# Kernel tuning notes

Measured on AMD Instinct MI355X. Metric: run time of the kernel, lower is better.

The kernel has to match this reference:

```python
import jax, jax.numpy as jnp
import numpy as np

# dims: D=embed_dim (= number of experts), H=heads, P=image patches, Q=query embeddings, B=batch
D, H, N, P, B, Q = 256, 8, 256, 1024, 1, 64
HD = D // H
EPS = 1e-5


def _ln(x, g, b):
    m = x.mean(-1, keepdims=True)
    v = x.var(-1, keepdims=True)
    return (x - m) / jnp.sqrt(v + EPS) * g + b


def _mha(q_x, kv_x, Wqkv, bqkv, Wo, bo):
    # standard torch nn.MultiheadAttention (batch_first, eval mode)
    Wq, Wk, Wv = jnp.split(Wqkv, 3, axis=0)
    bq, bk, bv = jnp.split(bqkv, 3, axis=0)
    q = q_x @ Wq.T + bq
    k = kv_x @ Wk.T + bk
    v = kv_x @ Wv.T + bv
    Bq, S, _ = q.shape
    Sk = k.shape[1]
    qh = q.reshape(Bq, S, H, HD)
    kh = k.reshape(Bq, Sk, H, HD)
    vh = v.reshape(Bq, Sk, H, HD)
    att = jax.nn.softmax(jnp.einsum('bqhd,bkhd->bhqk', qh, kh) / np.sqrt(HD).astype(np.float32), axis=-1)
    ctx = jnp.einsum('bhqk,bkhd->bqhd', att, vh).reshape(Bq, S, D)
    return ctx @ Wo.T + bo


def setup_inputs() -> dict:
    key = jax.random.key(0)
    ks = jax.random.split(key, 12)
    s = 0.02  # weight init scale
    return {
        'image_patches': jax.random.normal(ks[0], (B, P, D), jnp.float32),
        'expert_tokens': jax.random.normal(ks[1], (B, N, D), jnp.float32),
        'query_embeddings': jax.random.normal(ks[2], (B, Q, D), jnp.float32),
        'Wqkv_experts': jax.random.normal(ks[3], (N, 3 * D, D), jnp.float32) * s,
        'bqkv_experts': jnp.zeros((N, 3 * D), jnp.float32),
        'Wo_experts': jax.random.normal(ks[4], (N, D, D), jnp.float32) * s,
        'bo_experts': jnp.zeros((N, D), jnp.float32),
        'Wqkv_q': jax.random.normal(ks[5], (3 * D, D), jnp.float32) * s,
        'bqkv_q': jnp.zeros((3 * D,), jnp.float32),
        'Wo_q': jax.random.normal(ks[6], (D, D), jnp.float32) * s,
        'bo_q': jnp.zeros((D,), jnp.float32),
        'Wqkv_s': jax.random.normal(ks[7], (3 * D, D), jnp.float32) * s,
        'bqkv_s': jnp.zeros((3 * D,), jnp.float32),
        'Wo_s': jax.random.normal(ks[8], (D, D), jnp.float32) * s,
        'bo_s': jnp.zeros((D,), jnp.float32),
        'W1': jax.random.normal(ks[9], (4 * D, D), jnp.float32) * s,
        'b1': jnp.zeros((4 * D,), jnp.float32),
        'W2': jax.random.normal(ks[10], (D, 4 * D), jnp.float32) * s,
        'b2': jnp.zeros((D,), jnp.float32),
        'ln1_g': jnp.ones((D,), jnp.float32), 'ln1_b': jnp.zeros((D,), jnp.float32),
        'ln2_g': jnp.ones((D,), jnp.float32), 'ln2_b': jnp.zeros((D,), jnp.float32),
        'ln3_g': jnp.ones((D,), jnp.float32), 'ln3_b': jnp.zeros((D,), jnp.float32),
    }


def reference(image_patches, expert_tokens, query_embeddings,
              Wqkv_experts, bqkv_experts, Wo_experts, bo_experts,
              Wqkv_q, bqkv_q, Wo_q, bo_q,
              Wqkv_s, bqkv_s, Wo_s, bo_s,
              W1, b1, W2, b2,
              ln1_g, ln1_b, ln2_g, ln2_b, ln3_g, ln3_b):
    # --- per-expert cross attention (the embed_dim separate MHA calls, fused/batched) ---
    Wq, Wk, Wv = jnp.split(Wqkv_experts, 3, axis=1)   # each [N, D, D]
    bq, bk, bv = jnp.split(bqkv_experts, 3, axis=1)   # each [N, D]
    q = jnp.einsum('bnd,ned->bne', expert_tokens, Wq) + bq                       # [B,N,D]
    K = jnp.einsum('bpd,ned->bnpe', image_patches, Wk) + bk[None, :, None, :]    # [B,N,P,D]
    V = jnp.einsum('bpd,ned->bnpe', image_patches, Wv) + bv[None, :, None, :]    # [B,N,P,D]
    qh = q.reshape(B, N, H, HD)
    Kh = K.reshape(B, N, P, H, HD)
    Vh = V.reshape(B, N, P, H, HD)
    att = jax.nn.softmax(jnp.einsum('bnhd,bnphd->bnhp', qh, Kh) / np.sqrt(HD).astype(np.float32), axis=-1)
    image_attention_weights = att.mean(axis=2)        # [B,N,P] head-averaged, torch default
    ctx = jnp.einsum('bnhp,bnphd->bnhd', att, Vh).reshape(B, N, D)
    attended_image = jnp.einsum('bnd,ned->bne', ctx, Wo_experts) + bo_experts    # [B,N,D]
    attended_image = _ln(attended_image + expert_tokens, ln1_g, ln1_b)
    # --- query cross attention ---
    attended_query = _mha(attended_image, query_embeddings, Wqkv_q, bqkv_q, Wo_q, bo_q)
    attended_query = _ln(attended_query + attended_image, ln2_g, ln2_b)
    # --- FFN (no residual in original) ---
    expert_refined = jax.nn.relu(attended_query @ W1.T + b1) @ W2.T + b2
    # --- expert self attention + residual + norm ---
    sa = _mha(expert_refined, expert_refined, Wqkv_s, bqkv_s, Wo_s, bo_s)
    expert_features = _ln(sa + expert_refined, ln3_g, ln3_b)
    return expert_features, image_attention_weights
```

## Files before the change

kernel.cpp:

```cpp
#include <hip/hip_runtime.h>

#define DD 256
#define NH 8
#define NP 1024
#define NQ 64
#define SCALE 0.17677669529663687f

typedef float f32x4v __attribute__((ext_vector_type(4)));
typedef __bf16 bfv8 __attribute__((ext_vector_type(8)));

union BF8 { bfv8 v; unsigned short u16[8]; uint4 q; };

__device__ __forceinline__ float wred_sum(float p) {
  #pragma unroll
  for (int m = 32; m; m >>= 1) p += __shfl_xor(p, m);
  return p;
}
__device__ __forceinline__ float wred_max(float p) {
  #pragma unroll
  for (int m = 32; m; m >>= 1) p = fmaxf(p, __shfl_xor(p, m));
  return p;
}
__device__ __forceinline__ float red8(float p) {
  p += __shfl_xor(p, 1);
  p += __shfl_xor(p, 2);
  p += __shfl_xor(p, 4);
  return p;
}
__device__ __forceinline__ float dot4(float4 a, float4 b) {
  return a.x*b.x + a.y*b.y + a.z*b.z + a.w*b.w;
}
__device__ __forceinline__ unsigned short f2b(float f) {
  unsigned int u = __float_as_uint(f);
  u += 0x7fffu + ((u >> 16) & 1u);
  return (unsigned short)(u >> 16);
}
__device__ __forceinline__ BF8 cvt8(float4 a, float4 b) {
  BF8 r;
  r.u16[0]=f2b(a.x); r.u16[1]=f2b(a.y); r.u16[2]=f2b(a.z); r.u16[3]=f2b(a.w);
  r.u16[4]=f2b(b.x); r.u16[5]=f2b(b.y); r.u16[6]=f2b(b.z); r.u16[7]=f2b(b.w);
  return r;
}
__device__ __forceinline__ f32x4v mfma16(BF8 a, BF8 b, f32x4v c) {
  return __builtin_amdgcn_mfma_f32_16x16x32_bf16(a.v, b.v, c, 0, 0, 0);
}
__device__ __forceinline__ float2 b2f2(unsigned int u) {
  return make_float2(__uint_as_float(u << 16), __uint_as_float(u & 0xffff0000u));
}
__device__ __forceinline__ float dotb8(uint4 w, float4 x0, float4 x1) {
  float2 p0 = b2f2(w.x), p1 = b2f2(w.y), p2 = b2f2(w.z), p3 = b2f2(w.w);
  return p0.x*x0.x + p0.y*x0.y + p1.x*x0.z + p1.y*x0.w
       + p2.x*x1.x + p2.y*x1.y + p3.x*x1.z + p3.y*x1.w;
}

__device__ __forceinline__ void preload8(const float* x, int lane, float4* xf) {
  const int o = (lane & 7) * 4;
  #pragma unroll
  for (int cc = 0; cc < 8; ++cc) xf[cc] = *(const float4*)&x[cc*32 + o];
}
__device__ __forceinline__ void pass16(const float* __restrict__ W, int ldk,
                                       int r0, int lane, const float4* xf,
                                       float* outA, float* outB) {
  const float* baseA = W + (size_t)(r0 + (lane >> 3))*ldk + (lane & 7)*4;
  const float* baseB = baseA + (size_t)8*ldk;
  float4 wa[8], wb[8];
  #pragma unroll
  for (int cc = 0; cc < 8; ++cc) wa[cc] = *(const float4*)&baseA[cc*32];
  #pragma unroll
  for (int cc = 0; cc < 8; ++cc) wb[cc] = *(const float4*)&baseB[cc*32];
  float a = 0.f, b = 0.f;
  #pragma unroll
  for (int cc = 0; cc < 8; ++cc) { a += dot4(wa[cc], xf[cc]); b += dot4(wb[cc], xf[cc]); }
  *outA = red8(a); *outB = red8(b);
}
__device__ __forceinline__ void preload8b(const float* x, int lane, float4* xf) {
  const int o = (lane & 7) * 8;
  #pragma unroll
  for (int cc = 0; cc < 4; ++cc) {
    xf[2*cc]   = *(const float4*)&x[cc*64 + o];
    xf[2*cc+1] = *(const float4*)&x[cc*64 + o + 4];
  }
}
__device__ __forceinline__ void pass16b(const unsigned short* __restrict__ W, int ldk,
                                        int r0, int lane, const float4* xf,
                                        float* outA, float* outB) {
  const unsigned short* baseA = W + (size_t)(r0 + (lane >> 3))*ldk + (lane & 7)*8;
  const unsigned short* baseB = baseA + (size_t)8*ldk;
  uint4 wa[4], wb[4];
  #pragma unroll
  for (int cc = 0; cc < 4; ++cc) wa[cc] = *(const uint4*)&baseA[cc*64];
  #pragma unroll
  for (int cc = 0; cc < 4; ++cc) wb[cc] = *(const uint4*)&baseB[cc*64];
  float a = 0.f, b = 0.f;
  #pragma unroll
  for (int cc = 0; cc < 4; ++cc) {
    a += dotb8(wa[cc], xf[2*cc], xf[2*cc+1]);
    b += dotb8(wb[cc], xf[2*cc], xf[2*cc+1]);
  }
  *outA = red8(a); *outB = red8(b);
}

__device__ __forceinline__ void layernorm_store(const float* buf, float* outp,
                                                const float* g, const float* b,
                                                float* red, int tid, int wid, int lane)
{
  __syncthreads();
  if (wid == 0) {
    float s = buf[lane] + buf[lane+64] + buf[lane+128] + buf[lane+192];
    s = wred_sum(s);
    if (!lane) red[0] = s * (1.f/256.f);
  }
  __syncthreads();
  float mn = red[0];
  if (wid == 0) {
    float d0 = buf[lane]-mn, d1 = buf[lane+64]-mn, d2 = buf[lane+128]-mn, d3 = buf[lane+192]-mn;
    float s = d0*d0 + d1*d1 + d2*d2 + d3*d3;
    s = wred_sum(s);
    if (!lane) red[1] = rsqrtf(s * (1.f/256.f) + 1e-5f);
  }
  __syncthreads();
  if (tid < 256) outp[tid] = (buf[tid] - mn) * red[1] * g[tid] + b[tid];
}

__global__ __launch_bounds__(256)
void k_pre(const float* __restrict__ patches, uint4* __restrict__ pTB,
           uint4* __restrict__ patchesB,
           const float* __restrict__ qe, const float* __restrict__ Wqkv_q,
           const float* __restrict__ bqkv_q, float* __restrict__ kvq,
           const float* __restrict__ Wo_q, const float* __restrict__ W1,
           const float* __restrict__ W2, const float* __restrict__ Wqkv_s,
           unsigned short* __restrict__ wsB)
{
  const int b = blockIdx.x, tid = threadIdx.x;
  if (b < 128) {
    const int T = b*4 + (tid >> 6), l = tid & 63;
    const int kt = T >> 6, nt = T & 63;
    const int row = nt*16 + (l & 15), col = kt*32 + (l >> 4)*8;
    float4 a = *(const float4*)&patches[(size_t)row*DD + col];
    float4 c = *(const float4*)&patches[(size_t)row*DD + col + 4];
    pTB[(size_t)T*64 + l] = cvt8(a, c).q;
  } else if (b < 256) {
    const int T = (b - 128)*4 + (tid >> 6), l = tid & 63;
    const int kt = T >> 4, nt = T & 15;
    const int col = nt*16 + (l & 15), p0 = kt*32 + (l >> 4)*8;
    float v[8];
    #pragma unroll
    for (int j = 0; j < 8; ++j) v[j] = patches[(size_t)(p0 + j)*DD + col];
    BF8 r;
    #pragma unroll
    for (int j = 0; j < 8; ++j) r.u16[j] = f2b(v[j]);
    patchesB[(size_t)T*64 + l] = r.q;
  } else if (b < 320) {
    __shared__ float x[DD], kvrow[512];
    const int j = b - 256, w = tid >> 6, lane = tid & 63;
    if (tid < DD) x[tid] = qe[j*DD + tid];
    __syncthreads();
    float4 xf[8]; preload8(x, lane, xf);
    #pragma unroll
    for (int g = 0; g < 8; ++g) {
      int r0 = w*128 + g*16;
      float a, bb;
      pass16(Wqkv_q + (size_t)DD*DD, DD, r0, lane, xf, &a, &bb);
      int rA = r0 + (lane >> 3);
      if ((lane & 7) == 0) {
        kvrow[rA]   = a  + bqkv_q[DD + rA];
        kvrow[rA+8] = bb + bqkv_q[DD + rA + 8];
      }
    }
    __syncthreads();
    kvq[(size_t)j*512 + tid]       = kvrow[tid];
    kvq[(size_t)j*512 + 256 + tid] = kvrow[256 + tid];
  } else {
    const int gid = (b - 320)*256 + tid;
    const float* src;
    size_t dof;
    if      (gid < 8192)  { src = Wqkv_q + (size_t)gid*8;           dof = (size_t)gid*8; }
    else if (gid < 16384) { src = Wo_q   + (size_t)(gid-8192)*8;    dof = 65536  + (size_t)(gid-8192)*8; }
    else if (gid < 49152) { src = W1     + (size_t)(gid-16384)*8;   dof = 131072 + (size_t)(gid-16384)*8; }
    else if (gid < 81920) { src = W2     + (size_t)(gid-49152)*8;   dof = 393216 + (size_t)(gid-49152)*8; }
    else                  { src = Wqkv_s + (size_t)(gid-81920)*8;   dof = 655360 + (size_t)(gid-81920)*8; }
    float4 a = *(const float4*)&src[0];
    float4 c = *(const float4*)&src[4];
    *(uint4*)&wsB[dof] = cvt8(a, c).q;
  }
}

__global__ __launch_bounds__(256)
void k_qt(const float* __restrict__ et_g, const float* __restrict__ Wqkv_e,
          const float* __restrict__ bqkv_e, float* __restrict__ t_ws)
{
  const int b = blockIdx.x, n = b >> 2, hh = b & 3;
  const int tid = threadIdx.x, w = tid >> 6, lane = tid & 63;
  __shared__ float x[DD], qL[64], tpart[4][DD];
  const float* Wn = Wqkv_e + (size_t)n*(3*DD*DD);
  const float* bn = bqkv_e + (size_t)n*(3*DD);
  if (tid < DD) x[tid] = et_g[(size_t)n*DD + tid];
  __syncthreads();
  {
    float4 xf[8]; preload8(x, lane, xf);
    float a, bq;
    pass16(Wn, DD, hh*64 + w*16, lane, xf, &a, &bq);
    int rL = w*16 + (lane >> 3);
    if ((lane & 7) == 0) {
      qL[rL]   = a  + bn[hh*64 + rL];
      qL[rL+8] = bq + bn[hh*64 + rL + 8];
    }
  }
  __syncthreads();
  {
    const float* Wk = Wn + (size_t)DD*DD + (size_t)(hh*64 + w*16)*DD;
    float4 acc = make_float4(0.f, 0.f, 0.f, 0.f);
    #pragma unroll
    for (int r = 0; r < 16; ++r) {
      float qs = qL[w*16 + r];
      float4 wv = *(const float4*)&Wk[(size_t)r*DD + 4*lane];
      acc.x += qs*wv.x; acc.y += qs*wv.y; acc.z += qs*wv.z; acc.w += qs*wv.w;
    }
    *(float4*)&tpart[w][4*lane] = acc;
  }
  __syncthreads();
  {
    float tA = tpart[0][tid] + tpart[1][tid];
    float tB = tpart[2][tid] + tpart[3][tid];
    t_ws[(size_t)n*2048 + (size_t)(2*hh)*DD + tid]     = tA;
    t_ws[(size_t)n*2048 + (size_t)(2*hh+1)*DD + tid]   = tB;
  }
}

__global__ __launch_bounds__(512)
void k_mid1(const float* __restrict__ t_ws,
            const uint4* __restrict__ pTB, const uint4* __restrict__ patchesB,
            float* __restrict__ u_ws, float* __restrict__ iaw)
{
  const int n = blockIdx.x, tid = threadIdx.x, w = tid >> 6, lane = tid & 63;
  __shared__ float attS[NH][NP];
  __shared__ __align__(16) uint4 attB[16][128];
  __shared__ float tS[16][260];
  __shared__ float uS[NH][DD];

  for (int idx = tid; idx < 2048; idx += 512) tS[idx >> 8][idx & 255] = t_ws[(size_t)n*2048 + idx];
  __syncthreads();

  BF8 afr[8];
  {
    const int rr = lane & 15, ko = (lane >> 4)*8;
    #pragma unroll
    for (int kt = 0; kt < 8; ++kt) {
      float4 a = *(const float4*)&tS[rr][kt*32 + ko];
      float4 c = *(const float4*)&tS[rr][kt*32 + ko + 4];
      afr[kt] = cvt8(a, c);
    }
  }
  {
    #pragma unroll
    for (int t8 = 0; t8 < 8; ++t8) {
      const int nt = w*8 + t8;
      f32x4v acc = {0.f, 0.f, 0.f, 0.f};
      #pragma unroll
      for (int kt = 0; kt < 8; ++kt) {
        BF8 bb; bb.q = pTB[(size_t)(kt*64 + nt)*64 + lane];
        acc = mfma16(afr[kt], bb, acc);
      }
      if (lane < 32) {
        const int r0 = (lane >> 4)*4, cc = nt*16 + (lane & 15);
        #pragma unroll
        for (int i = 0; i < 4; ++i) attS[r0 + i][cc] = acc[i];
      }
    }
  }
  __syncthreads();
  {
    const int h = w;
    float v[16];
    #pragma unroll
    for (int k = 0; k < 16; ++k) v[k] = attS[h][k*64 + lane] * SCALE;
    float mx = v[0];
    #pragma unroll
    for (int k = 1; k < 16; ++k) mx = fmaxf(mx, v[k]);
    mx = wred_max(mx);
    float sum = 0.f;
    #pragma unroll
    for (int k = 0; k < 16; ++k) { v[k] = __expf(v[k] - mx); sum += v[k]; }
    sum = wred_sum(sum);
    float rinv = 1.f / sum;
    #pragma unroll
    for (int k = 0; k < 16; ++k) attS[h][k*64 + lane] = v[k] * rinv;
  }
  __syncthreads();
  #pragma unroll
  for (int rep = 0; rep < 2; ++rep) {
    int p = rep*512 + tid;
    float s = 0.f;
    #pragma unroll
    for (int h = 0; h < NH; ++h) s += attS[h][p];
    iaw[(size_t)n*NP + p] = s * 0.125f;
  }
  #pragma unroll
  for (int rep = 0; rep < 2; ++rep) {
    int C = rep*512 + tid;
    int row = C >> 7, c = C & 127;
    float4 a = *(const float4*)&attS[row][c*8];
    float4 b = *(const float4*)&attS[row][c*8 + 4];
    int swz = (c & ~7) | ((c ^ row) & 7);
    attB[row][swz] = cvt8(a, b).q;
  }
  __syncthreads();
  {
    const int nt0 = 2*w, nt1 = 2*w + 1;
    f32x4v acc0 = {0.f,0.f,0.f,0.f}, acc1 = {0.f,0.f,0.f,0.f};
    const int rr = lane & 15, cq = lane >> 4;
    #pragma unroll 8
    for (int kt = 0; kt < 32; ++kt) {
      int cc = kt*4 + cq;
      int swz = (cc & ~7) | ((cc ^ rr) & 7);
      BF8 a;  a.q  = attB[rr][swz];
      BF8 b0; b0.q = patchesB[(size_t)(kt*16 + nt0)*64 + lane];
      BF8 b1; b1.q = patchesB[(size_t)(kt*16 + nt1)*64 + lane];
      acc0 = mfma16(a, b0, acc0);
      acc1 = mfma16(a, b1, acc1);
    }
    if (lane < 32) {
      const int r0 = (lane >> 4)*4;
      #pragma unroll
      for (int i = 0; i < 4; ++i) {
        uS[r0+i][nt0*16 + (lane & 15)] = acc0[i];
        uS[r0+i][nt1*16 + (lane & 15)] = acc1[i];
      }
    }
  }
  __syncthreads();
  for (int idx = tid; idx < 2048; idx += 512) u_ws[(size_t)n*2048 + idx] = (&uS[0][0])[idx];
}

__global__ __launch_bounds__(256)
void k_ctx(const float* __restrict__ u_ws, const float* __restrict__ Wqkv_e,
           const float* __restrict__ bqkv_e, float* __restrict__ ctx_ws)
{
  const int b = blockIdx.x, n = b >> 2, qt = b & 3;
  const int tid = threadIdx.x, w = tid >> 6, lane = tid & 63;
  const float* Wn = Wqkv_e + (size_t)n*(3*DD*DD);
  const float* bn = bqkv_e + (size_t)n*(3*DD);
  const int head = qt*2 + (w >> 1);
  float4 xf[8]; preload8(u_ws + (size_t)n*2048 + (size_t)head*DD, lane, xf);
  float a, bq;
  pass16(Wn + (size_t)2*DD*DD, DD, qt*64 + w*16, lane, xf, &a, &bq);
  int rA = qt*64 + w*16 + (lane >> 3);
  if ((lane & 7) == 0) {
    ctx_ws[(size_t)n*DD + rA]     = a  + bn[2*DD + rA];
    ctx_ws[(size_t)n*DD + rA + 8] = bq + bn[2*DD + rA + 8];
  }
}

__global__ __launch_bounds__(256)
void k_out(const float* __restrict__ ctx_ws, const float* __restrict__ et_g,
           const float* __restrict__ Wo_e, const float* __restrict__ bo_e,
           float* __restrict__ res_ws)
{
  const int b = blockIdx.x, n = b >> 2, qt = b & 3;
  const int tid = threadIdx.x, w = tid >> 6, lane = tid & 63;
  __shared__ float cx[DD];
  if (tid < DD) cx[tid] = ctx_ws[(size_t)n*DD + tid];
  __syncthreads();
  float4 xf[8]; preload8(cx, lane, xf);
  float a, bq;
  pass16(Wo_e + (size_t)n*DD*DD, DD, qt*64 + w*16, lane, xf, &a, &bq);
  int rA = qt*64 + w*16 + (lane >> 3);
  if ((lane & 7) == 0) {
    res_ws[(size_t)n*DD + rA]     = a  + bo_e[(size_t)n*DD + rA]     + et_g[(size_t)n*DD + rA];
    res_ws[(size_t)n*DD + rA + 8] = bq + bo_e[(size_t)n*DD + rA + 8] + et_g[(size_t)n*DD + rA + 8];
  }
}

__global__ __launch_bounds__(1024)
void k_tail(const float* __restrict__ res_ws, const float* __restrict__ kvq,
            const unsigned short* __restrict__ wsB,
            const float* __restrict__ bqkv_q, const float* __restrict__ bo_q,
            const float* __restrict__ b1, const float* __restrict__ b2,
            const float* __restrict__ bqkv_s,
            const float* __restrict__ ln1g, const float* __restrict__ ln1b,
            const float* __restrict__ ln2g, const float* __restrict__ ln2b,
            float* __restrict__ er_g, float* __restrict__ qkvs_g)
{
  const int n = blockIdx.x, tid = threadIdx.x, w = tid >> 6, lane = tid & 63;
  __shared__ float xL[DD], qL[DD], ctxL[DD], resS[DD], attq[NH][NQ], red2[2];
  __shared__ float hb[1024], qrow[768];
  const unsigned short* WqB  = wsB;
  const unsigned short* WoqB = wsB + 65536;
  const unsigned short* W1B  = wsB + 131072;
  const unsigned short* W2B  = wsB + 393216;
  const unsigned short* WsB  = wsB + 655360;

  if (tid < DD) resS[tid] = res_ws[(size_t)n*DD + tid];
  layernorm_store(resS, xL, ln1g, ln1b, red2, tid, w, lane);
  __syncthreads();

  {
    float4 xf[8]; preload8b(xL, lane, xf);
    float a, b;
    pass16b(WqB, DD, w*16, lane, xf, &a, &b);
    int rA = w*16 + (lane >> 3);
    if ((lane & 7) == 0) { qL[rA] = a + bqkv_q[rA]; qL[rA+8] = b + bqkv_q[rA+8]; }
  }
  __syncthreads();
  if (w < 8) {
    const int h = w, j = lane;
    float4 q4[8];
    #pragma unroll
    for (int m = 0; m < 8; ++m) q4[m] = *(const float4*)&qL[h*32 + 4*m];
    const float* kj = kvq + (size_t)j*512 + h*32;
    float s = 0.f;
    #pragma unroll
    for (int m = 0; m < 8; ++m) s += dot4(*(const float4*)&kj[4*m], q4[m]);
    s *= SCALE;
    float mx = wred_max(s);
    float p = __expf(s - mx);
    float sum = wred_sum(p);
    attq[h][j] = p / sum;
  }
  __syncthreads();
  if (tid < DD) {
    const int rr = tid, h = rr >> 5;
    float acc = 0.f;
    #pragma unroll 4
    for (int j4 = 0; j4 < 16; ++j4) {
      float4 a4 = *(const float4*)&attq[h][j4*4];
      acc += a4.x * kvq[(size_t)(j4*4+0)*512 + DD + rr]
           + a4.y * kvq[(size_t)(j4*4+1)*512 + DD + rr]
           + a4.z * kvq[(size_t)(j4*4+2)*512 + DD + rr]
           + a4.w * kvq[(size_t)(j4*4+3)*512 + DD + rr];
    }
    ctxL[rr] = acc;
  }
  __syncthreads();
  {
    float4 xf[8]; preload8b(ctxL, lane, xf);
    float a, b;
    pass16b(WoqB, DD, w*16, lane, xf, &a, &b);
    int rA = w*16 + (lane >> 3);
    if ((lane & 7) == 0) { resS[rA] = a + bo_q[rA] + xL[rA]; resS[rA+8] = b + bo_q[rA+8] + xL[rA+8]; }
  }
  layernorm_store(resS, xL, ln2g, ln2b, red2, tid, w, lane);
  __syncthreads();

  {
    float4 xf[8]; preload8b(xL, lane, xf);
    #pragma unroll
    for (int g = 0; g < 4; ++g) {
      int r0 = w*64 + g*16;
      float a, b;
      pass16b(W1B, DD, r0, lane, xf, &a, &b);
      int rA = r0 + (lane >> 3);
      if ((lane & 7) == 0) { hb[rA] = fmaxf(a + b1[rA], 0.f); hb[rA+8] = fmaxf(b + b1[rA+8], 0.f); }
    }
  }
  __syncthreads();
  {
    float accA = 0.f, accB = 0.f;
    #pragma unroll
    for (int kc = 0; kc < 4; ++kc) {
      float4 xh[8]; preload8b(hb + kc*256, lane, xh);
      float a, b;
      pass16b(W2B + kc*256, 1024, w*16, lane, xh, &a, &b);
      accA += a; accB += b;
    }
    int rA = w*16 + (lane >> 3);
    if ((lane & 7) == 0) { qL[rA] = accA + b2[rA]; qL[rA+8] = accB + b2[rA+8]; }
  }
  __syncthreads();
  {
    float4 xf[8]; preload8b(qL, lane, xf);
    #pragma unroll
    for (int g = 0; g < 3; ++g) {
      int r0 = w*48 + g*16;
      float a, b;
      pass16b(WsB, DD, r0, lane, xf, &a, &b);
      int rA = r0 + (lane >> 3);
      if ((lane & 7) == 0) { qrow[rA] = a + bqkv_s[rA]; qrow[rA+8] = b + bqkv_s[rA+8]; }
    }
  }
  __syncthreads();
  if (tid < 768) qkvs_g[(size_t)n*768 + tid] = qrow[tid];
  if (tid < DD)  er_g[(size_t)n*DD + tid]   = qL[tid];
}

__global__ __launch_bounds__(1024)
void k_sa(const float* __restrict__ er, const float* __restrict__ qkvs,
          const float* __restrict__ Wo_s, const float* __restrict__ bo_s,
          const float* __restrict__ ln3g, const float* __restrict__ ln3b,
          float* __restrict__ ef)
{
  const int i = blockIdx.x, tid = threadIdx.x, w = tid >> 6, lane = tid & 63;
  __shared__ float x[DD], attl[NH][256], ctxp[4][DD], resS[DD], red2[2];
  if (tid < DD) x[tid] = er[(size_t)i*DD + tid];
  {
    const int h = w & 7, kh = w >> 3;
    float4 q4[8];
    #pragma unroll
    for (int m = 0; m < 8; ++m) q4[m] = *(const float4*)&qkvs[(size_t)i*768 + h*32 + 4*m];
    #pragma unroll
    for (int rep = 0; rep < 2; ++rep) {
      int j = kh*128 + rep*64 + lane;
      const float* kj = qkvs + (size_t)j*768 + DD + h*32;
      float4 k4[8];
      #pragma unroll
      for (int m = 0; m < 8; ++m) k4[m] = *(const float4*)&kj[4*m];
      float s = 0.f;
      #pragma unroll
      for (int m = 0; m < 8; ++m) s += dot4(k4[m], q4[m]);
      attl[h][j] = s * SCALE;
    }
  }
  __syncthreads();
  if (w < 8) {
    const int h = w;
    float v0 = attl[h][lane], v1 = attl[h][lane+64], v2 = attl[h][lane+128], v3 = attl[h][lane+192];
    float mx = wred_max(fmaxf(fmaxf(v0,v1), fmaxf(v2,v3)));
    float e0 = __expf(v0-mx), e1 = __expf(v1-mx), e2 = __expf(v2-mx), e3 = __expf(v3-mx);
    float sum = wred_sum(e0+e1+e2+e3);
    float r = 1.f/sum;
    attl[h][lane] = e0*r; attl[h][lane+64] = e1*r; attl[h][lane+128] = e2*r; attl[h][lane+192] = e3*r;
  }
  __syncthreads();
  {
    const int rr = tid & 255, qtr = tid >> 8, h = rr >> 5;
    float acc = 0.f;
    #pragma unroll 4
    for (int j4 = qtr*16; j4 < qtr*16 + 16; ++j4) {
      float4 a4 = *(const float4*)&attl[h][j4*4];
      acc += a4.x * qkvs[(size_t)(j4*4+0)*768 + 512 + rr]
           + a4.y * qkvs[(size_t)(j4*4+1)*768 + 512 + rr]
           + a4.z * qkvs[(size_t)(j4*4+2)*768 + 512 + rr]
           + a4.w * qkvs[(size_t)(j4*4+3)*768 + 512 + rr];
    }
    ctxp[qtr][rr] = acc;
  }
  __syncthreads();
  {
    float4 xf[8];
    const int o = (lane & 7)*4;
    #pragma unroll
    for (int cc = 0; cc < 8; ++cc) {
      float4 a = *(const float4*)&ctxp[0][cc*32 + o];
      float4 b = *(const float4*)&ctxp[1][cc*32 + o];
      float4 c = *(const float4*)&ctxp[2][cc*32 + o];
      float4 d = *(const float4*)&ctxp[3][cc*32 + o];
      xf[cc] = make_float4(a.x+b.x+c.x+d.x, a.y+b.y+c.y+d.y,
                           a.z+b.z+c.z+d.z, a.w+b.w+c.w+d.w);
    }
    float a, b;
    pass16(Wo_s, DD, w*16, lane, xf, &a, &b);
    int rA = w*16 + (lane >> 3);
    if ((lane & 7) == 0) { resS[rA] = a + bo_s[rA] + x[rA]; resS[rA+8] = b + bo_s[rA+8] + x[rA+8]; }
  }
  layernorm_store(resS, ef + (size_t)i*DD, ln3g, ln3b, red2, tid, w, lane);
}

extern "C" void kernel_launch(void* const* d_in, const int* in_sizes, int n_in,
                              void* d_out, int out_size, void* d_ws, size_t ws_size,
                              hipStream_t stream) {
  const float* patches = (const float*)d_in[0];
  const float* et      = (const float*)d_in[1];
  const float* qe      = (const float*)d_in[2];
  const float* Wqkv_e  = (const float*)d_in[3];
  const float* bqkv_e  = (const float*)d_in[4];
  const float* Wo_e    = (const float*)d_in[5];
  const float* bo_e    = (const float*)d_in[6];
  const float* Wqkv_q  = (const float*)d_in[7];
  const float* bqkv_q  = (const float*)d_in[8];
  const float* Wo_q    = (const float*)d_in[9];
  const float* bo_q    = (const float*)d_in[10];
  const float* Wqkv_s  = (const float*)d_in[11];
  const float* bqkv_s  = (const float*)d_in[12];
  const float* Wo_s    = (const float*)d_in[13];
  const float* bo_s    = (const float*)d_in[14];
  const float* W1      = (const float*)d_in[15];
  const float* b1      = (const float*)d_in[16];
  const float* W2      = (const float*)d_in[17];
  const float* b2      = (const float*)d_in[18];
  const float* ln1g = (const float*)d_in[19]; const float* ln1b = (const float*)d_in[20];
  const float* ln2g = (const float*)d_in[21]; const float* ln2b = (const float*)d_in[22];
  const float* ln3g = (const float*)d_in[23]; const float* ln3b = (const float*)d_in[24];

  float* ef  = (float*)d_out;
  float* iaw = (float*)d_out + 65536;

  float* ws           = (float*)d_ws;
  uint4* pTB          = (uint4*)ws;
  uint4* patchesB     = (uint4*)(ws + 131072);
  float* kvq          = ws + 262144;
  float* t_ws         = ws + 294912;
  float* u_ws         = ws + 819200;
  float* ctx_ws       = ws + 1343488;
  float* res_ws       = ws + 1409024;
  float* er           = ws + 1474560;
  float* qkvs         = ws + 1540096;
  unsigned short* wsB = (unsigned short*)(ws + 1736704);

  k_pre<<<736, 256, 0, stream>>>(patches, pTB, patchesB, qe, Wqkv_q, bqkv_q, kvq,
                                 Wo_q, W1, W2, Wqkv_s, wsB);
  k_qt<<<1024, 256, 0, stream>>>(et, Wqkv_e, bqkv_e, t_ws);
  k_mid1<<<256, 512, 0, stream>>>(t_ws, pTB, patchesB, u_ws, iaw);
  k_ctx<<<1024, 256, 0, stream>>>(u_ws, Wqkv_e, bqkv_e, ctx_ws);
  k_out<<<1024, 256, 0, stream>>>(ctx_ws, et, Wo_e, bo_e, res_ws);
  k_tail<<<256, 1024, 0, stream>>>(res_ws, kvq, wsB, bqkv_q, bo_q, b1, b2, bqkv_s,
                                   ln1g, ln1b, ln2g, ln2b, er, qkvs);
  k_sa<<<256, 1024, 0, stream>>>(er, qkvs, Wo_s, bo_s, ln3g, ln3b, ef);
}
```

Baseline: 145.9 us.

## Fuse expert q/t, attention and ctx kernels into one two-block-per-expert kernel

Merges k_qt, k_mid1 and k_ctx into a single k_front2 kernel. Each expert is split across two 512-thread blocks, one per group of four heads, so the t and u intermediates stay in shared memory instead of going through global workspace. Shared memory is reused through an aliased buffer, and the head-averaged attention weights are written as per-half partials that k_tail combines. This removes two kernel launches and the global round trips, at the cost of some wasted MFMA rows (only 4 of 16 used) and an extra partial-sum pass.

```diff
diff --git a/kernel.cpp b/kernel.cpp
--- a/kernel.cpp
+++ b/kernel.cpp
@@ -185,60 +185,59 @@
   }
 }
 
-__global__ __launch_bounds__(256)
-void k_qt(const float* __restrict__ et_g, const float* __restrict__ Wqkv_e,
-          const float* __restrict__ bqkv_e, float* __restrict__ t_ws)
+__global__ __launch_bounds__(512, 4)
+void k_front2(const float* __restrict__ et_g,
+              const float* __restrict__ Wqkv_e, const float* __restrict__ bqkv_e,
+              const uint4* __restrict__ pTB, const uint4* __restrict__ patchesB,
+              float* __restrict__ ctx_ws, float* __restrict__ iawp)
 {
-  const int b = blockIdx.x, n = b >> 2, hh = b & 3;
+  const int blk = blockIdx.x, n = blk >> 1, half = blk & 1;
   const int tid = threadIdx.x, w = tid >> 6, lane = tid & 63;
-  __shared__ float x[DD], qL[64], tpart[4][DD];
+  __shared__ __align__(16) char big[32768];
+  __shared__ float attS[4][NP];
+  __shared__ float uS[4][DD];
+  __shared__ float xL[DD], qL[128];
+  float (*tpart)[256] = (float (*)[256])big;
+  float (*tS)[260]    = (float (*)[260])(big + 8192);
+  uint4 (*attB)[128]  = (uint4 (*)[128])big;
+
   const float* Wn = Wqkv_e + (size_t)n*(3*DD*DD);
   const float* bn = bqkv_e + (size_t)n*(3*DD);
-  if (tid < DD) x[tid] = et_g[(size_t)n*DD + tid];
-  __syncthreads();
-  {
-    float4 xf[8]; preload8(x, lane, xf);
+
+  if (tid < DD) xL[tid] = et_g[(size_t)n*DD + tid];
+  __syncthreads();
+
+  {
+    float4 xf[8]; preload8(xL, lane, xf);
     float a, bq;
-    pass16(Wn, DD, hh*64 + w*16, lane, xf, &a, &bq);
+    pass16(Wn, DD, half*128 + w*16, lane, xf, &a, &bq);
     int rL = w*16 + (lane >> 3);
     if ((lane & 7) == 0) {
-      qL[rL]   = a  + bn[hh*64 + rL];
-      qL[rL+8] = bq + bn[hh*64 + rL + 8];
-    }
-  }
-  __syncthreads();
-  {
-    const float* Wk = Wn + (size_t)DD*DD + (size_t)(hh*64 + w*16)*DD;
+      qL[rL]   = a  + bn[half*128 + rL];
+      qL[rL+8] = bq + bn[half*128 + rL + 8];
+    }
+  }
+  __syncthreads();
+
+  {
+    const int hl = w >> 1, dh = w & 1;
+    const float* Wk = Wn + (size_t)DD*DD + (size_t)(half*128 + hl*32 + dh*16)*DD;
     float4 acc = make_float4(0.f, 0.f, 0.f, 0.f);
     #pragma unroll
     for (int r = 0; r < 16; ++r) {
-      float qs = qL[w*16 + r];
+      float qs = qL[hl*32 + dh*16 + r];
       float4 wv = *(const float4*)&Wk[(size_t)r*DD + 4*lane];
       acc.x += qs*wv.x; acc.y += qs*wv.y; acc.z += qs*wv.z; acc.w += qs*wv.w;
     }
     *(float4*)&tpart[w][4*lane] = acc;
   }
   __syncthreads();
-  {
-    float tA = tpart[0][tid] + tpart[1][tid];
-    float tB = tpart[2][tid] + tpart[3][tid];
-    t_ws[(size_t)n*2048 + (size_t)(2*hh)*DD + tid]     = tA;
-    t_ws[(size_t)n*2048 + (size_t)(2*hh+1)*DD + tid]   = tB;
-  }
-}
-
-__global__ __launch_bounds__(512)
-void k_mid1(const float* __restrict__ t_ws,
-            const uint4* __restrict__ pTB, const uint4* __restrict__ patchesB,
-            float* __restrict__ u_ws, float* __restrict__ iaw)
-{
-  const int n = blockIdx.x, tid = threadIdx.x, w = tid >> 6, lane = tid & 63;
-  __shared__ float attS[NH][NP];
-  __shared__ __align__(16) uint4 attB[16][128];
-  __shared__ float tS[16][260];
-  __shared__ float uS[NH][DD];
-
-  for (int idx = tid; idx < 2048; idx += 512) tS[idx >> 8][idx & 255] = t_ws[(size_t)n*2048 + idx];
+  #pragma unroll
+  for (int rep = 0; rep < 2; ++rep) {
+    int idx = rep*512 + tid;
+    int hl = idx >> 8, c = idx & 255;
+    tS[hl][c] = tpart[2*hl][c] + tpart[2*hl+1][c];
+  }
   __syncthreads();
 
   BF8 afr[8];
@@ -261,19 +260,20 @@
         BF8 bb; bb.q = pTB[(size_t)(kt*64 + nt)*64 + lane];
         acc = mfma16(afr[kt], bb, acc);
       }
-      if (lane < 32) {
-        const int r0 = (lane >> 4)*4, cc = nt*16 + (lane & 15);
+      if (lane < 16) {
+        const int cc = nt*16 + lane;
         #pragma unroll
-        for (int i = 0; i < 4; ++i) attS[r0 + i][cc] = acc[i];
+        for (int i = 0; i < 4; ++i) attS[i][cc] = acc[i];
       }
     }
   }
   __syncthreads();
-  {
-    const int h = w;
+
+  if (w < 4) {
+    const int hl = w;
     float v[16];
     #pragma unroll
-    for (int k = 0; k < 16; ++k) v[k] = attS[h][k*64 + lane] * SCALE;
+    for (int k = 0; k < 16; ++k) v[k] = attS[hl][k*64 + lane] * SCALE;
     float mx = v[0];
     #pragma unroll
     for (int k = 1; k < 16; ++k) mx = fmaxf(mx, v[k]);
@@ -284,27 +284,25 @@
     sum = wred_sum(sum);
     float rinv = 1.f / sum;
     #pragma unroll
-    for (int k = 0; k < 16; ++k) attS[h][k*64 + lane] = v[k] * rinv;
-  }
-  __syncthreads();
+    for (int k = 0; k < 16; ++k) attS[hl][k*64 + lane] = v[k] * rinv;
+  }
+  __syncthreads();
+
   #pragma unroll
   for (int rep = 0; rep < 2; ++rep) {
     int p = rep*512 + tid;
-    float s = 0.f;
-    #pragma unroll
-    for (int h = 0; h < NH; ++h) s += attS[h][p];
-    iaw[(size_t)n*NP + p] = s * 0.125f;
-  }
-  #pragma unroll
-  for (int rep = 0; rep < 2; ++rep) {
-    int C = rep*512 + tid;
-    int row = C >> 7, c = C & 127;
+    float s = attS[0][p] + attS[1][p] + attS[2][p] + attS[3][p];
+    iawp[(size_t)blk*NP + p] = s;
+  }
+  {
+    int row = tid >> 7, c = tid & 127;
     float4 a = *(const float4*)&attS[row][c*8];
     float4 b = *(const float4*)&attS[row][c*8 + 4];
     int swz = (c & ~7) | ((c ^ row) & 7);
     attB[row][swz] = cvt8(a, b).q;
   }
   __syncthreads();
+
   {
     const int nt0 = 2*w, nt1 = 2*w + 1;
     f32x4v acc0 = {0.f,0.f,0.f,0.f}, acc1 = {0.f,0.f,0.f,0.f};
@@ -319,39 +317,30 @@
       acc0 = mfma16(a, b0, acc0);
       acc1 = mfma16(a, b1, acc1);
     }
-    if (lane < 32) {
-      const int r0 = (lane >> 4)*4;
+    if (lane < 16) {
       #pragma unroll
       for (int i = 0; i < 4; ++i) {
-        uS[r0+i][nt0*16 + (lane & 15)] = acc0[i];
-        uS[r0+i][nt1*16 + (lane & 15)] = acc1[i];
+        uS[i][nt0*16 + lane] = acc0[i];
+        uS[i][nt1*16 + lane] = acc1[i];
       }
     }
   }
   __syncthreads();
-  for (int idx = tid; idx < 2048; idx += 512) u_ws[(size_t)n*2048 + idx] = (&uS[0][0])[idx];
-}
-
-__global__ __launch_bounds__(256)
-void k_ctx(const float* __restrict__ u_ws, const float* __restrict__ Wqkv_e,
-           const float* __restrict__ bqkv_e, float* __restrict__ ctx_ws)
-{
-  const int b = blockIdx.x, n = b >> 2, qt = b & 3;
-  const int tid = threadIdx.x, w = tid >> 6, lane = tid & 63;
-  const float* Wn = Wqkv_e + (size_t)n*(3*DD*DD);
-  const float* bn = bqkv_e + (size_t)n*(3*DD);
-  const int head = qt*2 + (w >> 1);
-  float4 xf[8]; preload8(u_ws + (size_t)n*2048 + (size_t)head*DD, lane, xf);
-  float a, bq;
-  pass16(Wn + (size_t)2*DD*DD, DD, qt*64 + w*16, lane, xf, &a, &bq);
-  int rA = qt*64 + w*16 + (lane >> 3);
-  if ((lane & 7) == 0) {
-    ctx_ws[(size_t)n*DD + rA]     = a  + bn[2*DD + rA];
-    ctx_ws[(size_t)n*DD + rA + 8] = bq + bn[2*DD + rA + 8];
-  }
-}
-
-__global__ __launch_bounds__(256)
+
+  {
+    const int hl = w >> 1;
+    float4 xf[8]; preload8(&uS[hl][0], lane, xf);
+    float a, bq;
+    pass16(Wn + (size_t)2*DD*DD, DD, half*128 + w*16, lane, xf, &a, &bq);
+    int rA = half*128 + w*16 + (lane >> 3);
+    if ((lane & 7) == 0) {
+      ctx_ws[(size_t)n*DD + rA]     = a  + bn[2*DD + rA];
+      ctx_ws[(size_t)n*DD + rA + 8] = bq + bn[2*DD + rA + 8];
+    }
+  }
+}
+
+__global__ __launch_bounds__(256, 6)
 void k_out(const float* __restrict__ ctx_ws, const float* __restrict__ et_g,
            const float* __restrict__ Wo_e, const float* __restrict__ bo_e,
            float* __restrict__ res_ws)
@@ -373,13 +362,15 @@
 
 __global__ __launch_bounds__(1024)
 void k_tail(const float* __restrict__ res_ws, const float* __restrict__ kvq,
+            const float* __restrict__ iawp,
             const unsigned short* __restrict__ wsB,
             const float* __restrict__ bqkv_q, const float* __restrict__ bo_q,
             const float* __restrict__ b1, const float* __restrict__ b2,
             const float* __restrict__ bqkv_s,
             const float* __restrict__ ln1g, const float* __restrict__ ln1b,
             const float* __restrict__ ln2g, const float* __restrict__ ln2b,
-            float* __restrict__ er_g, float* __restrict__ qkvs_g)
+            float* __restrict__ er_g, float* __restrict__ qkvs_g,
+            float* __restrict__ iaw)
 {
   const int n = blockIdx.x, tid = threadIdx.x, w = tid >> 6, lane = tid & 63;
   __shared__ float xL[DD], qL[DD], ctxL[DD], resS[DD], attq[NH][NQ], red2[2];
@@ -389,6 +380,9 @@
   const unsigned short* W1B  = wsB + 131072;
   const unsigned short* W2B  = wsB + 393216;
   const unsigned short* WsB  = wsB + 655360;
+
+  iaw[(size_t)n*NP + tid] = 0.125f *
+    (iawp[(size_t)(2*n)*NP + tid] + iawp[(size_t)(2*n+1)*NP + tid]);
 
   if (tid < DD) resS[tid] = res_ws[(size_t)n*DD + tid];
   layernorm_store(resS, xL, ln1g, ln1b, red2, tid, w, lane);
@@ -588,21 +582,18 @@
   uint4* pTB          = (uint4*)ws;
   uint4* patchesB     = (uint4*)(ws + 131072);
   float* kvq          = ws + 262144;
-  float* t_ws         = ws + 294912;
-  float* u_ws         = ws + 819200;
-  float* ctx_ws       = ws + 1343488;
-  float* res_ws       = ws + 1409024;
-  float* er           = ws + 1474560;
-  float* qkvs         = ws + 1540096;
-  unsigned short* wsB = (unsigned short*)(ws + 1736704);
+  float* iawp         = ws + 294912;
+  float* ctx_ws       = ws + 819200;
+  float* res_ws       = ws + 884736;
+  float* er           = ws + 950272;
+  float* qkvs         = ws + 1015808;
+  unsigned short* wsB = (unsigned short*)(ws + 1212416);
 
   k_pre<<<736, 256, 0, stream>>>(patches, pTB, patchesB, qe, Wqkv_q, bqkv_q, kvq,
                                  Wo_q, W1, W2, Wqkv_s, wsB);
-  k_qt<<<1024, 256, 0, stream>>>(et, Wqkv_e, bqkv_e, t_ws);
-  k_mid1<<<256, 512, 0, stream>>>(t_ws, pTB, patchesB, u_ws, iaw);
-  k_ctx<<<1024, 256, 0, stream>>>(u_ws, Wqkv_e, bqkv_e, ctx_ws);
+  k_front2<<<512, 512, 0, stream>>>(et, Wqkv_e, bqkv_e, pTB, patchesB, ctx_ws, iawp);
   k_out<<<1024, 256, 0, stream>>>(ctx_ws, et, Wo_e, bo_e, res_ws);
-  k_tail<<<256, 1024, 0, stream>>>(res_ws, kvq, wsB, bqkv_q, bo_q, b1, b2, bqkv_s,
-                                   ln1g, ln1b, ln2g, ln2b, er, qkvs);
+  k_tail<<<256, 1024, 0, stream>>>(res_ws, kvq, iawp, wsB, bqkv_q, bo_q, b1, b2, bqkv_s,
+                                   ln1g, ln1b, ln2g, ln2b, er, qkvs, iaw);
   k_sa<<<256, 1024, 0, stream>>>(er, qkvs, Wo_s, bo_s, ln3g, ln3b, ef);
 }
```

After: 139.5 us. -4.4%, faster.

## Split q/t expert projections into separate kernels with per-wave row GEMVs

Applied to the files above, without the earlier changes.

Replaces the fused k_qt kernel with two kernels: k_q computes the expert query vector with each wave handling 16 weight rows, issuing all 16 float4 loads up front and reducing with wave shuffles. k_t then computes the per-head key projection from the stored q. k_ctx and k_out are rewritten in the same per-wave 16-row style, which drops shared memory and __syncthreads. The aim is more memory-level parallelism on the large per-expert weight streams. The cost is an extra kernel launch and a round trip of q through global memory.

```diff
diff --git a/kernel.cpp b/kernel.cpp
--- a/kernel.cpp
+++ b/kernel.cpp
@@ -186,45 +186,44 @@
 }
 
 __global__ __launch_bounds__(256)
-void k_qt(const float* __restrict__ et_g, const float* __restrict__ Wqkv_e,
-          const float* __restrict__ bqkv_e, float* __restrict__ t_ws)
-{
-  const int b = blockIdx.x, n = b >> 2, hh = b & 3;
-  const int tid = threadIdx.x, w = tid >> 6, lane = tid & 63;
-  __shared__ float x[DD], qL[64], tpart[4][DD];
-  const float* Wn = Wqkv_e + (size_t)n*(3*DD*DD);
-  const float* bn = bqkv_e + (size_t)n*(3*DD);
-  if (tid < DD) x[tid] = et_g[(size_t)n*DD + tid];
-  __syncthreads();
-  {
-    float4 xf[8]; preload8(x, lane, xf);
-    float a, bq;
-    pass16(Wn, DD, hh*64 + w*16, lane, xf, &a, &bq);
-    int rL = w*16 + (lane >> 3);
-    if ((lane & 7) == 0) {
-      qL[rL]   = a  + bn[hh*64 + rL];
-      qL[rL+8] = bq + bn[hh*64 + rL + 8];
-    }
-  }
-  __syncthreads();
-  {
-    const float* Wk = Wn + (size_t)DD*DD + (size_t)(hh*64 + w*16)*DD;
-    float4 acc = make_float4(0.f, 0.f, 0.f, 0.f);
-    #pragma unroll
-    for (int r = 0; r < 16; ++r) {
-      float qs = qL[w*16 + r];
-      float4 wv = *(const float4*)&Wk[(size_t)r*DD + 4*lane];
-      acc.x += qs*wv.x; acc.y += qs*wv.y; acc.z += qs*wv.z; acc.w += qs*wv.w;
-    }
-    *(float4*)&tpart[w][4*lane] = acc;
-  }
-  __syncthreads();
-  {
-    float tA = tpart[0][tid] + tpart[1][tid];
-    float tB = tpart[2][tid] + tpart[3][tid];
-    t_ws[(size_t)n*2048 + (size_t)(2*hh)*DD + tid]     = tA;
-    t_ws[(size_t)n*2048 + (size_t)(2*hh+1)*DD + tid]   = tB;
-  }
+void k_q(const float* __restrict__ et_g, const float* __restrict__ Wqkv_e,
+         const float* __restrict__ bqkv_e, float* __restrict__ q_ws)
+{
+  const int gw = (blockIdx.x*256 + threadIdx.x) >> 6;
+  const int lane = threadIdx.x & 63;
+  const int g0 = gw * 16, n = g0 >> 8, r0 = g0 & 255;
+  const float* W = Wqkv_e + (size_t)n*(3*DD*DD) + (size_t)r0*DD + 4*lane;
+  float4 x4 = *(const float4*)&et_g[(size_t)n*DD + 4*lane];
+  float4 wv[16];
+  #pragma unroll
+  for (int r = 0; r < 16; ++r) wv[r] = *(const float4*)&W[(size_t)r*DD];
+  float s[16];
+  #pragma unroll
+  for (int r = 0; r < 16; ++r) s[r] = wred_sum(dot4(wv[r], x4));
+  if (lane == 0) {
+    #pragma unroll
+    for (int r = 0; r < 16; ++r)
+      q_ws[(size_t)n*DD + r0 + r] = s[r] + bqkv_e[(size_t)n*768 + r0 + r];
+  }
+}
+
+__global__ __launch_bounds__(256)
+void k_t(const float* __restrict__ q_ws, const float* __restrict__ Wqkv_e,
+         float* __restrict__ t_ws)
+{
+  const int gw = (blockIdx.x*256 + threadIdx.x) >> 6;
+  const int lane = threadIdx.x & 63;
+  const int n = gw >> 3, h = gw & 7;
+  const float* Wk = Wqkv_e + (size_t)n*(3*DD*DD) + (size_t)DD*DD + (size_t)(h*32)*DD + 4*lane;
+  const float* q  = q_ws + (size_t)n*DD + h*32;
+  float4 acc = make_float4(0.f, 0.f, 0.f, 0.f);
+  #pragma unroll
+  for (int r = 0; r < 32; ++r) {
+    float qs = q[r];
+    float4 wvv = *(const float4*)&Wk[(size_t)r*DD];
+    acc.x += qs*wvv.x; acc.y += qs*wvv.y; acc.z += qs*wvv.z; acc.w += qs*wvv.w;
+  }
+  *(float4*)&t_ws[(size_t)n*2048 + h*256 + 4*lane] = acc;
 }
 
 __global__ __launch_bounds__(512)
@@ -336,18 +335,21 @@
 void k_ctx(const float* __restrict__ u_ws, const float* __restrict__ Wqkv_e,
            const float* __restrict__ bqkv_e, float* __restrict__ ctx_ws)
 {
-  const int b = blockIdx.x, n = b >> 2, qt = b & 3;
-  const int tid = threadIdx.x, w = tid >> 6, lane = tid & 63;
-  const float* Wn = Wqkv_e + (size_t)n*(3*DD*DD);
-  const float* bn = bqkv_e + (size_t)n*(3*DD);
-  const int head = qt*2 + (w >> 1);
-  float4 xf[8]; preload8(u_ws + (size_t)n*2048 + (size_t)head*DD, lane, xf);
-  float a, bq;
-  pass16(Wn + (size_t)2*DD*DD, DD, qt*64 + w*16, lane, xf, &a, &bq);
-  int rA = qt*64 + w*16 + (lane >> 3);
-  if ((lane & 7) == 0) {
-    ctx_ws[(size_t)n*DD + rA]     = a  + bn[2*DD + rA];
-    ctx_ws[(size_t)n*DD + rA + 8] = bq + bn[2*DD + rA + 8];
+  const int gw = (blockIdx.x*256 + threadIdx.x) >> 6;
+  const int lane = threadIdx.x & 63;
+  const int g0 = gw * 16, n = g0 >> 8, r0 = g0 & 255, head = r0 >> 5;
+  const float* W = Wqkv_e + (size_t)n*(3*DD*DD) + (size_t)2*DD*DD + (size_t)r0*DD + 4*lane;
+  float4 x4 = *(const float4*)&u_ws[(size_t)n*2048 + head*256 + 4*lane];
+  float4 wv[16];
+  #pragma unroll
+  for (int r = 0; r < 16; ++r) wv[r] = *(const float4*)&W[(size_t)r*DD];
+  float s[16];
+  #pragma unroll
+  for (int r = 0; r < 16; ++r) s[r] = wred_sum(dot4(wv[r], x4));
+  if (lane == 0) {
+    #pragma unroll
+    for (int r = 0; r < 16; ++r)
+      ctx_ws[(size_t)n*DD + r0 + r] = s[r] + bqkv_e[(size_t)n*768 + 2*DD + r0 + r];
   }
 }
 
@@ -356,18 +358,22 @@
            const float* __restrict__ Wo_e, const float* __restrict__ bo_e,
            float* __restrict__ res_ws)
 {
-  const int b = blockIdx.x, n = b >> 2, qt = b & 3;
-  const int tid = threadIdx.x, w = tid >> 6, lane = tid & 63;
-  __shared__ float cx[DD];
-  if (tid < DD) cx[tid] = ctx_ws[(size_t)n*DD + tid];
-  __syncthreads();
-  float4 xf[8]; preload8(cx, lane, xf);
-  float a, bq;
-  pass16(Wo_e + (size_t)n*DD*DD, DD, qt*64 + w*16, lane, xf, &a, &bq);
-  int rA = qt*64 + w*16 + (lane >> 3);
-  if ((lane & 7) == 0) {
-    res_ws[(size_t)n*DD + rA]     = a  + bo_e[(size_t)n*DD + rA]     + et_g[(size_t)n*DD + rA];
-    res_ws[(size_t)n*DD + rA + 8] = bq + bo_e[(size_t)n*DD + rA + 8] + et_g[(size_t)n*DD + rA + 8];
+  const int gw = (blockIdx.x*256 + threadIdx.x) >> 6;
+  const int lane = threadIdx.x & 63;
+  const int g0 = gw * 16, n = g0 >> 8, r0 = g0 & 255;
+  const float* W = Wo_e + (size_t)n*DD*DD + (size_t)r0*DD + 4*lane;
+  float4 x4 = *(const float4*)&ctx_ws[(size_t)n*DD + 4*lane];
+  float4 wv[16];
+  #pragma unroll
+  for (int r = 0; r < 16; ++r) wv[r] = *(const float4*)&W[(size_t)r*DD];
+  float s[16];
+  #pragma unroll
+  for (int r = 0; r < 16; ++r) s[r] = wred_sum(dot4(wv[r], x4));
+  if (lane == 0) {
+    #pragma unroll
+    for (int r = 0; r < 16; ++r)
+      res_ws[(size_t)n*DD + r0 + r] = s[r] + bo_e[(size_t)n*DD + r0 + r]
+                                           + et_g[(size_t)n*DD + r0 + r];
   }
 }
 
@@ -588,17 +594,19 @@
   uint4* pTB          = (uint4*)ws;
   uint4* patchesB     = (uint4*)(ws + 131072);
   float* kvq          = ws + 262144;
-  float* t_ws         = ws + 294912;
-  float* u_ws         = ws + 819200;
-  float* ctx_ws       = ws + 1343488;
-  float* res_ws       = ws + 1409024;
-  float* er           = ws + 1474560;
-  float* qkvs         = ws + 1540096;
-  unsigned short* wsB = (unsigned short*)(ws + 1736704);
+  float* q_ws         = ws + 294912;
+  float* t_ws         = ws + 360448;
+  float* u_ws         = ws + 884736;
+  float* ctx_ws       = ws + 1409024;
+  float* res_ws       = ws + 1474560;
+  float* er           = ws + 1540096;
+  float* qkvs         = ws + 1605632;
+  unsigned short* wsB = (unsigned short*)(ws + 1802240);
 
   k_pre<<<736, 256, 0, stream>>>(patches, pTB, patchesB, qe, Wqkv_q, bqkv_q, kvq,
                                  Wo_q, W1, W2, Wqkv_s, wsB);
-  k_qt<<<1024, 256, 0, stream>>>(et, Wqkv_e, bqkv_e, t_ws);
+  k_q<<<1024, 256, 0, stream>>>(et, Wqkv_e, bqkv_e, q_ws);
+  k_t<<<512, 256, 0, stream>>>(q_ws, Wqkv_e, t_ws);
   k_mid1<<<256, 512, 0, stream>>>(t_ws, pTB, patchesB, u_ws, iaw);
   k_ctx<<<1024, 256, 0, stream>>>(u_ws, Wqkv_e, bqkv_e, ctx_ws);
   k_out<<<1024, 256, 0, stream>>>(ctx_ws, et, Wo_e, bo_e, res_ws);
```

Measured after the change: 150.7 us. +3.3%, slower.
